# Kernel optimization log

Hardware: AMD Instinct MI355X
Metric: run time of the kernel (lower is better)

The kernel has to match this reference:

```python
import jax, jax.numpy as jnp
import numpy as np

LR = 0.1          # RMSprop learning rate (set_hyper_parameters)
ALPHA = 0.9       # RMSprop decay
ITERATIONS = 5    # SVGD iterations
INV_SIG2 = 1.0    # Gaussian posterior score scale (concrete post_grad)
EPS = 1e-8


def setup_inputs() -> dict:
    key = jax.random.key(0)
    k1, k2 = jax.random.split(key)
    x = jax.random.normal(k1, (8, 2048, 8), dtype=jnp.float32)          # [B, N, D] particles
    observation = jax.random.normal(k2, (8, 8), dtype=jnp.float32)      # [B, D]
    return {"x": x, "observation": observation}


def _svgd(x, observation):
    B, N, D = x.shape
    # median heuristic bandwidth h = median(pairwise dist)^2 / log(N), per batch, no-grad
    sq = jnp.sum((x[:, :, None, :] - x[:, None, :, :]) ** 2, axis=-1)   # [B, N, N]
    med = jnp.median(jnp.sqrt(sq).reshape(B, -1), axis=-1)              # [B]
    h = jax.lax.stop_gradient(med ** 2 / jnp.log(jnp.float32(N)))       # [B]
    inv_N = jnp.float32(1.0 / N)

    def post_grad(xc):
        # Gaussian posterior score: d/dx log N(x; observation, sigma^2 I)
        return (observation[:, None, :] - xc) * INV_SIG2                # [B, N, D]

    def step(carry, _):
        xc, s = carry
        dist = xc[:, :, None, :] - xc[:, None, :, :]                    # [B, i, j, D]
        K = jnp.exp(-jnp.sum(dist ** 2, axis=-1) / h[:, None, None])    # [B, i, j] rbf
        g = post_grad(xc)                                               # [B, j, D]
        # phi_i = (1/N) sum_j [ K_ij * g_j + (2/h)(x_i - x_j) K_ij ]
        phi = inv_N * (jnp.einsum('bij,bjd->bid', K, g)
                       + (2.0 / h)[:, None, None] * jnp.einsum('bij,bijd->bid', K, dist))
        # RMSprop (state update under no_grad in the original)
        s = jax.lax.stop_gradient(ALPHA * s + (1.0 - ALPHA) * phi ** 2)
        xc = xc + LR * phi / (jnp.sqrt(s) + EPS)
        return (xc, s), None

    (x, _), _ = jax.lax.scan(step, (x, jnp.zeros_like(x)), None, length=ITERATIONS)
    return x


def reference(x, observation):
    return _svgd(x, observation)
```

## Files before the change

kernel.cpp:

```cpp
#include <hip/hip_runtime.h>
#include <cstdint>

#define BATCH 8
#define NPART 2048
#define DDIM 8
#define NN (NPART * NPART)

#define MJCHUNK 256
#define SJCHUNK 512

constexpr float LR = 0.1f;
constexpr float ALPHA = 0.9f;
constexpr float EPS = 1e-8f;
constexpr float INV_N = 1.0f / (float)NPART;

typedef float v2f __attribute__((ext_vector_type(2)));
typedef float v4f __attribute__((ext_vector_type(4)));

__global__ __launch_bounds__(256) void init_ws_k(float* __restrict__ s,
                                                 unsigned* __restrict__ hist,
                                                 unsigned* __restrict__ prefix,
                                                 unsigned* __restrict__ rank) {
    const int tid = blockIdx.x * 256 + threadIdx.x;
    const int stride = gridDim.x * 256;
    for (int q = tid; q < BATCH * NPART * DDIM; q += stride) s[q] = 0.0f;
    if (tid < BATCH * 2 * 256) hist[tid] = 0u;
    if (tid < BATCH * 2) {
        prefix[tid] = 0u;
        rank[tid] = (unsigned)(NN / 2) + (unsigned)(tid & 1);
    }
}

__global__ __launch_bounds__(256) void median_hist_k(const float* __restrict__ x,
                                                     unsigned* __restrict__ hist,
                                                     const unsigned* __restrict__ prefix,
                                                     int shift) {
    __shared__ __align__(16) v4f xs0[MJCHUNK];
    __shared__ __align__(16) v4f xs1[MJCHUNK];
    __shared__ float rs[MJCHUNK];
    __shared__ unsigned lh[256 * 32];

    const int b = blockIdx.x;
    const int tid = threadIdx.x;
    const int slot = tid & 31;
    const float* xb = x + (size_t)b * NPART * DDIM;

    const unsigned p0 = prefix[2 * b + 0];
    const unsigned p1 = prefix[2 * b + 1];
    const bool same = (p0 == p1);
    const unsigned mask = (shift == 24) ? 0u : (0xFFFFFFFFu << (shift + 8));

    const int lane = tid & 15;
    const int trow = tid >> 4;
    const int ia = blockIdx.y * 32 + trow;
    const int ib = ia + 16;

    const v4f a0 = ((const v4f*)(xb + (size_t)ia * DDIM))[0];
    const v4f a1 = ((const v4f*)(xb + (size_t)ia * DDIM))[1];
    const v4f b0 = ((const v4f*)(xb + (size_t)ib * DDIM))[0];
    const v4f b1 = ((const v4f*)(xb + (size_t)ib * DDIM))[1];
    float qa = a0.x * a0.x + a0.y * a0.y + a0.z * a0.z + a0.w * a0.w
             + a1.x * a1.x + a1.y * a1.y + a1.z * a1.z + a1.w * a1.w;
    float qb = b0.x * b0.x + b0.y * b0.y + b0.z * b0.z + b0.w * b0.w
             + b1.x * b1.x + b1.y * b1.y + b1.z * b1.z + b1.w * b1.w;

    const int nsel = same ? 1 : 2;
    for (int sel = 0; sel < nsel; ++sel) {
        const unsigned pref = sel ? p1 : p0;
        __syncthreads();
        for (int t = tid; t < 256 * 32; t += 256) lh[t] = 0u;

        for (int cbase = 0; cbase < NPART; cbase += MJCHUNK) {
            __syncthreads();
            for (int t = tid; t < MJCHUNK; t += 256) {
                const v4f u0 = ((const v4f*)(xb + (size_t)(cbase + t) * DDIM))[0];
                const v4f u1 = ((const v4f*)(xb + (size_t)(cbase + t) * DDIM))[1];
                xs0[t] = u0;
                xs1[t] = u1;
                rs[t] = u0.x * u0.x + u0.y * u0.y + u0.z * u0.z + u0.w * u0.w
                      + u1.x * u1.x + u1.y * u1.y + u1.z * u1.z + u1.w * u1.w;
            }
            __syncthreads();
#pragma unroll 4
            for (int j = lane; j < MJCHUNK; j += 16) {
                const v4f A = xs0[j];
                const v4f B = xs1[j];
                const float r = rs[j];
                const v2f A0 = A.xy, A1 = A.zw, B0 = B.xy, B1 = B.zw;
                v2f p = A0 * a0.xy;
                p += A1 * a0.zw;
                p += B0 * a1.xy;
                p += B1 * a1.zw;
                float sq = fmaxf(fmaf(-2.0f, p.x + p.y, qa + r), 0.0f);
                unsigned u = __float_as_uint(sq);
                if ((u & mask) == pref)
                    atomicAdd(&lh[((u >> shift) & 255u) * 32 + slot], 1u);
                v2f q = A0 * b0.xy;
                q += A1 * b0.zw;
                q += B0 * b1.xy;
                q += B1 * b1.zw;
                sq = fmaxf(fmaf(-2.0f, q.x + q.y, qb + r), 0.0f);
                u = __float_as_uint(sq);
                if ((u & mask) == pref)
                    atomicAdd(&lh[((u >> shift) & 255u) * 32 + slot], 1u);
            }
        }
        __syncthreads();
        unsigned tot = 0;
#pragma unroll
        for (int sct = 0; sct < 32; ++sct) tot += lh[tid * 32 + ((sct + tid) & 31)];
        if (tot) {
            atomicAdd(&hist[b * 512 + sel * 256 + tid], tot);
            if (same) atomicAdd(&hist[b * 512 + 256 + tid], tot);
        }
    }
}

__global__ void median_scan_k(unsigned* __restrict__ hist,
                              unsigned* __restrict__ prefix,
                              unsigned* __restrict__ rank,
                              int shift,
                              float* __restrict__ hpar) {
    __shared__ unsigned selv[16];
    const int t = threadIdx.x;
    if (t < 16) {
        const unsigned r = rank[t];
        const unsigned* hb = hist + t * 256;
        unsigned cum = 0;
        int bin = 0;
        for (; bin < 256; ++bin) {
            const unsigned c = hb[bin];
            if (cum + c >= r) break;
            cum += c;
        }
        if (bin > 255) bin = 255;
        const unsigned np = prefix[t] | ((unsigned)bin << shift);
        prefix[t] = np;
        rank[t] = r - cum;
        selv[t] = np;
    }
    __syncthreads();
    for (int q = t; q < 16 * 256; q += 64) hist[q] = 0u;
    if (shift == 8 && t < BATCH) {
        const float v1 = __uint_as_float(selv[2 * t + 0]);
        const float v2 = __uint_as_float(selv[2 * t + 1]);
        const float med = 0.5f * (sqrtf(v1) + sqrtf(v2));
        const float h = (med * med) / logf((float)NPART);
        hpar[2 * t + 0] = -1.0f / h;
        hpar[2 * t + 1] = 2.0f / h;
    }
}

__global__ __launch_bounds__(256) void svgd_step_k(const float* __restrict__ x_in,
                                                   float* __restrict__ x_out,
                                                   float* __restrict__ s,
                                                   const float* __restrict__ hpar,
                                                   const float* __restrict__ obs) {
    __shared__ __align__(16) v4f xs0[SJCHUNK];
    __shared__ __align__(16) v4f xs1[SJCHUNK];
    __shared__ float rs[SJCHUNK];
    __shared__ float part[32][16][9];

    const int b = blockIdx.x;
    const int tid = threadIdx.x;
    const float* xb = x_in + (size_t)b * NPART * DDIM;

    const float nih = hpar[2 * b + 0];
    const float c2 = hpar[2 * b + 1];
    const float cdot = -2.0f * nih;

    const int lane = tid & 15;
    const int trow = tid >> 4;
    const int ia = blockIdx.y * 32 + trow;
    const int ib = ia + 16;

    const v4f a0 = ((const v4f*)(xb + (size_t)ia * DDIM))[0];
    const v4f a1 = ((const v4f*)(xb + (size_t)ia * DDIM))[1];
    const v4f b0 = ((const v4f*)(xb + (size_t)ib * DDIM))[0];
    const v4f b1 = ((const v4f*)(xb + (size_t)ib * DDIM))[1];
    const float qa = nih * (a0.x * a0.x + a0.y * a0.y + a0.z * a0.z + a0.w * a0.w
                          + a1.x * a1.x + a1.y * a1.y + a1.z * a1.z + a1.w * a1.w);
    const float qb = nih * (b0.x * b0.x + b0.y * b0.y + b0.z * b0.z + b0.w * b0.w
                          + b1.x * b1.x + b1.y * b1.y + b1.z * b1.z + b1.w * b1.w);

    float S0a = 0.0f, S0b = 0.0f;
    v2f Va0 = {0, 0}, Va1 = {0, 0}, Va2 = {0, 0}, Va3 = {0, 0};
    v2f Vb0 = {0, 0}, Vb1 = {0, 0}, Vb2 = {0, 0}, Vb3 = {0, 0};

    for (int cbase = 0; cbase < NPART; cbase += SJCHUNK) {
        __syncthreads();
        for (int t = tid; t < SJCHUNK; t += 256) {
            const v4f u0 = ((const v4f*)(xb + (size_t)(cbase + t) * DDIM))[0];
            const v4f u1 = ((const v4f*)(xb + (size_t)(cbase + t) * DDIM))[1];
            xs0[t] = u0;
            xs1[t] = u1;
            rs[t] = nih * (u0.x * u0.x + u0.y * u0.y + u0.z * u0.z + u0.w * u0.w
                         + u1.x * u1.x + u1.y * u1.y + u1.z * u1.z + u1.w * u1.w);
        }
        __syncthreads();
#pragma unroll 4
        for (int j = lane; j < SJCHUNK; j += 16) {
            const v4f A = xs0[j];
            const v4f B = xs1[j];
            const float r = rs[j];
            const v2f A0 = A.xy, A1 = A.zw, B0 = B.xy, B1 = B.zw;
            v2f p = A0 * a0.xy;
            p += A1 * a0.zw;
            p += B0 * a1.xy;
            p += B1 * a1.zw;
            const float Ka = __expf(fmaf(cdot, p.x + p.y, qa + r));
            S0a += Ka;
            const v2f Ka2 = {Ka, Ka};
            Va0 += A0 * Ka2;
            Va1 += A1 * Ka2;
            Va2 += B0 * Ka2;
            Va3 += B1 * Ka2;
            v2f q = A0 * b0.xy;
            q += A1 * b0.zw;
            q += B0 * b1.xy;
            q += B1 * b1.zw;
            const float Kb = __expf(fmaf(cdot, q.x + q.y, qb + r));
            S0b += Kb;
            const v2f Kb2 = {Kb, Kb};
            Vb0 += A0 * Kb2;
            Vb1 += A1 * Kb2;
            Vb2 += B0 * Kb2;
            Vb3 += B1 * Kb2;
        }
    }
    part[trow][lane][0] = S0a;
    part[trow][lane][1] = Va0.x;
    part[trow][lane][2] = Va0.y;
    part[trow][lane][3] = Va1.x;
    part[trow][lane][4] = Va1.y;
    part[trow][lane][5] = Va2.x;
    part[trow][lane][6] = Va2.y;
    part[trow][lane][7] = Va3.x;
    part[trow][lane][8] = Va3.y;
    part[trow + 16][lane][0] = S0b;
    part[trow + 16][lane][1] = Vb0.x;
    part[trow + 16][lane][2] = Vb0.y;
    part[trow + 16][lane][3] = Vb1.x;
    part[trow + 16][lane][4] = Vb1.y;
    part[trow + 16][lane][5] = Vb2.x;
    part[trow + 16][lane][6] = Vb2.y;
    part[trow + 16][lane][7] = Vb3.x;
    part[trow + 16][lane][8] = Vb3.y;
    __syncthreads();

    {
        const int d2i = tid & 7;
        const int r2 = tid >> 3;
        const int i2 = blockIdx.y * 32 + r2;
        float S0t = 0.0f, Vt = 0.0f;
#pragma unroll
        for (int l = 0; l < 16; ++l) {
            S0t += part[r2][l][0];
            Vt += part[r2][l][1 + d2i];
        }
        const size_t idx = ((size_t)b * NPART + i2) * DDIM + d2i;
        const float xid = x_in[idx];
        const float obsd = obs[b * DDIM + d2i];
        const float U = fmaf(S0t, xid, -Vt);
        const float T = fmaf(S0t, obsd - xid, U);
        const float phi = INV_N * fmaf(c2, U, T);
        float sv = s[idx];
        sv = ALPHA * sv + (1.0f - ALPHA) * phi * phi;
        s[idx] = sv;
        x_out[idx] = xid + LR * phi / (sqrtf(sv) + EPS);
    }
}

extern "C" void kernel_launch(void* const* d_in, const int* in_sizes, int n_in,
                              void* d_out, int out_size, void* d_ws, size_t ws_size,
                              hipStream_t stream) {
    const float* x0 = (const float*)d_in[0];
    const float* obs = (const float*)d_in[1];
    float* out = (float*)d_out;

    float* xa = (float*)d_ws;
    float* s = xa + BATCH * NPART * DDIM;
    unsigned* hist = (unsigned*)(s + BATCH * NPART * DDIM);
    unsigned* prefix = hist + BATCH * 2 * 256;
    unsigned* rank = prefix + BATCH * 2;
    float* hpar = (float*)(rank + BATCH * 2);

    init_ws_k<<<256, 256, 0, stream>>>(s, hist, prefix, rank);

    for (int r = 0; r < 3; ++r) {
        const int shift = 24 - 8 * r;
        median_hist_k<<<dim3(BATCH, 64), 256, 0, stream>>>(x0, hist, prefix, shift);
        median_scan_k<<<1, 64, 0, stream>>>(hist, prefix, rank, shift, hpar);
    }

    svgd_step_k<<<dim3(BATCH, 64), 256, 0, stream>>>(x0, out, s, hpar, obs);
    svgd_step_k<<<dim3(BATCH, 64), 256, 0, stream>>>(out, xa, s, hpar, obs);
    svgd_step_k<<<dim3(BATCH, 64), 256, 0, stream>>>(xa, out, s, hpar, obs);
    svgd_step_k<<<dim3(BATCH, 64), 256, 0, stream>>>(out, xa, s, hpar, obs);
    svgd_step_k<<<dim3(BATCH, 64), 256, 0, stream>>>(xa, out, s, hpar, obs);
}
```

Baseline: 230.0 us.

## Register-block four rows per thread in median and SVGD kernels, skip s zeroing

Each thread now holds four query particles in registers and strides the shared j-chunk by 32 lanes instead of two rows with 16 lanes. Every shared-memory load of a j particle is therefore reused across four i rows, which cuts LDS traffic per pair computed. The first SVGD step also starts RMSprop from zero state instead of reading s, so the init kernel no longer has to clear s. The cost is more registers per thread (16 accumulators of v2f plus xi) and a larger partial-reduction buffer in shared memory, which may lower occupancy.

Result: no change. 231.0 us (+0.4%).

```diff
diff --git a/kernel.cpp b/kernel.cpp
--- a/kernel.cpp
+++ b/kernel.cpp
@@ -17,13 +17,10 @@
 typedef float v2f __attribute__((ext_vector_type(2)));
 typedef float v4f __attribute__((ext_vector_type(4)));
 
-__global__ __launch_bounds__(256) void init_ws_k(float* __restrict__ s,
-                                                 unsigned* __restrict__ hist,
+__global__ __launch_bounds__(256) void init_ws_k(unsigned* __restrict__ hist,
                                                  unsigned* __restrict__ prefix,
                                                  unsigned* __restrict__ rank) {
     const int tid = blockIdx.x * 256 + threadIdx.x;
-    const int stride = gridDim.x * 256;
-    for (int q = tid; q < BATCH * NPART * DDIM; q += stride) s[q] = 0.0f;
     if (tid < BATCH * 2 * 256) hist[tid] = 0u;
     if (tid < BATCH * 2) {
         prefix[tid] = 0u;
@@ -42,7 +39,8 @@
 
     const int b = blockIdx.x;
     const int tid = threadIdx.x;
-    const int slot = tid & 31;
+    const int lane = tid & 31;
+    const int trow = tid >> 5;
     const float* xb = x + (size_t)b * NPART * DDIM;
 
     const unsigned p0 = prefix[2 * b + 0];
@@ -50,19 +48,18 @@
     const bool same = (p0 == p1);
     const unsigned mask = (shift == 24) ? 0u : (0xFFFFFFFFu << (shift + 8));
 
-    const int lane = tid & 15;
-    const int trow = tid >> 4;
-    const int ia = blockIdx.y * 32 + trow;
-    const int ib = ia + 16;
-
-    const v4f a0 = ((const v4f*)(xb + (size_t)ia * DDIM))[0];
-    const v4f a1 = ((const v4f*)(xb + (size_t)ia * DDIM))[1];
-    const v4f b0 = ((const v4f*)(xb + (size_t)ib * DDIM))[0];
-    const v4f b1 = ((const v4f*)(xb + (size_t)ib * DDIM))[1];
-    float qa = a0.x * a0.x + a0.y * a0.y + a0.z * a0.z + a0.w * a0.w
-             + a1.x * a1.x + a1.y * a1.y + a1.z * a1.z + a1.w * a1.w;
-    float qb = b0.x * b0.x + b0.y * b0.y + b0.z * b0.z + b0.w * b0.w
-             + b1.x * b1.x + b1.y * b1.y + b1.z * b1.z + b1.w * b1.w;
+    const int ibase = blockIdx.y * 32 + trow * 4;
+    v2f xi[4][4];
+    float q[4];
+#pragma unroll
+    for (int rr = 0; rr < 4; ++rr) {
+        const v4f t0 = ((const v4f*)(xb + (size_t)(ibase + rr) * DDIM))[0];
+        const v4f t1 = ((const v4f*)(xb + (size_t)(ibase + rr) * DDIM))[1];
+        xi[rr][0] = t0.xy; xi[rr][1] = t0.zw;
+        xi[rr][2] = t1.xy; xi[rr][3] = t1.zw;
+        q[rr] = t0.x * t0.x + t0.y * t0.y + t0.z * t0.z + t0.w * t0.w
+              + t1.x * t1.x + t1.y * t1.y + t1.z * t1.z + t1.w * t1.w;
+    }
 
     const int nsel = same ? 1 : 2;
     for (int sel = 0; sel < nsel; ++sel) {
@@ -81,28 +78,23 @@
                       + u1.x * u1.x + u1.y * u1.y + u1.z * u1.z + u1.w * u1.w;
             }
             __syncthreads();
-#pragma unroll 4
-            for (int j = lane; j < MJCHUNK; j += 16) {
+#pragma unroll 2
+            for (int j = lane; j < MJCHUNK; j += 32) {
                 const v4f A = xs0[j];
                 const v4f B = xs1[j];
                 const float r = rs[j];
                 const v2f A0 = A.xy, A1 = A.zw, B0 = B.xy, B1 = B.zw;
-                v2f p = A0 * a0.xy;
-                p += A1 * a0.zw;
-                p += B0 * a1.xy;
-                p += B1 * a1.zw;
-                float sq = fmaxf(fmaf(-2.0f, p.x + p.y, qa + r), 0.0f);
-                unsigned u = __float_as_uint(sq);
-                if ((u & mask) == pref)
-                    atomicAdd(&lh[((u >> shift) & 255u) * 32 + slot], 1u);
-                v2f q = A0 * b0.xy;
-                q += A1 * b0.zw;
-                q += B0 * b1.xy;
-                q += B1 * b1.zw;
-                sq = fmaxf(fmaf(-2.0f, q.x + q.y, qb + r), 0.0f);
-                u = __float_as_uint(sq);
-                if ((u & mask) == pref)
-                    atomicAdd(&lh[((u >> shift) & 255u) * 32 + slot], 1u);
+#pragma unroll
+                for (int rr = 0; rr < 4; ++rr) {
+                    v2f p = A0 * xi[rr][0];
+                    p += A1 * xi[rr][1];
+                    p += B0 * xi[rr][2];
+                    p += B1 * xi[rr][3];
+                    const float sq = fmaxf(fmaf(-2.0f, p.x + p.y, q[rr] + r), 0.0f);
+                    const unsigned u = __float_as_uint(sq);
+                    if ((u & mask) == pref)
+                        atomicAdd(&lh[((u >> shift) & 255u) * 32 + lane], 1u);
+                }
             }
         }
         __syncthreads();
@@ -155,37 +147,42 @@
                                                    float* __restrict__ x_out,
                                                    float* __restrict__ s,
                                                    const float* __restrict__ hpar,
-                                                   const float* __restrict__ obs) {
+                                                   const float* __restrict__ obs,
+                                                   int first) {
     __shared__ __align__(16) v4f xs0[SJCHUNK];
     __shared__ __align__(16) v4f xs1[SJCHUNK];
     __shared__ float rs[SJCHUNK];
-    __shared__ float part[32][16][9];
+    __shared__ float part[32][32][9];
 
     const int b = blockIdx.x;
     const int tid = threadIdx.x;
+    const int lane = tid & 31;
+    const int trow = tid >> 5;
     const float* xb = x_in + (size_t)b * NPART * DDIM;
 
     const float nih = hpar[2 * b + 0];
     const float c2 = hpar[2 * b + 1];
     const float cdot = -2.0f * nih;
 
-    const int lane = tid & 15;
-    const int trow = tid >> 4;
-    const int ia = blockIdx.y * 32 + trow;
-    const int ib = ia + 16;
-
-    const v4f a0 = ((const v4f*)(xb + (size_t)ia * DDIM))[0];
-    const v4f a1 = ((const v4f*)(xb + (size_t)ia * DDIM))[1];
-    const v4f b0 = ((const v4f*)(xb + (size_t)ib * DDIM))[0];
-    const v4f b1 = ((const v4f*)(xb + (size_t)ib * DDIM))[1];
-    const float qa = nih * (a0.x * a0.x + a0.y * a0.y + a0.z * a0.z + a0.w * a0.w
-                          + a1.x * a1.x + a1.y * a1.y + a1.z * a1.z + a1.w * a1.w);
-    const float qb = nih * (b0.x * b0.x + b0.y * b0.y + b0.z * b0.z + b0.w * b0.w
-                          + b1.x * b1.x + b1.y * b1.y + b1.z * b1.z + b1.w * b1.w);
-
-    float S0a = 0.0f, S0b = 0.0f;
-    v2f Va0 = {0, 0}, Va1 = {0, 0}, Va2 = {0, 0}, Va3 = {0, 0};
-    v2f Vb0 = {0, 0}, Vb1 = {0, 0}, Vb2 = {0, 0}, Vb3 = {0, 0};
+    const int ibase = blockIdx.y * 32 + trow * 4;
+    v2f xi[4][4];
+    float q[4];
+#pragma unroll
+    for (int rr = 0; rr < 4; ++rr) {
+        const v4f t0 = ((const v4f*)(xb + (size_t)(ibase + rr) * DDIM))[0];
+        const v4f t1 = ((const v4f*)(xb + (size_t)(ibase + rr) * DDIM))[1];
+        xi[rr][0] = t0.xy; xi[rr][1] = t0.zw;
+        xi[rr][2] = t1.xy; xi[rr][3] = t1.zw;
+        q[rr] = nih * (t0.x * t0.x + t0.y * t0.y + t0.z * t0.z + t0.w * t0.w
+                     + t1.x * t1.x + t1.y * t1.y + t1.z * t1.z + t1.w * t1.w);
+    }
+
+    float S0[4] = {0, 0, 0, 0};
+    v2f V[4][4];
+#pragma unroll
+    for (int rr = 0; rr < 4; ++rr)
+#pragma unroll
+        for (int k = 0; k < 4; ++k) V[rr][k] = (v2f){0, 0};
 
     for (int cbase = 0; cbase < NPART; cbase += SJCHUNK) {
         __syncthreads();
@@ -198,54 +195,41 @@
                          + u1.x * u1.x + u1.y * u1.y + u1.z * u1.z + u1.w * u1.w);
         }
         __syncthreads();
-#pragma unroll 4
-        for (int j = lane; j < SJCHUNK; j += 16) {
+#pragma unroll 2
+        for (int j = lane; j < SJCHUNK; j += 32) {
             const v4f A = xs0[j];
             const v4f B = xs1[j];
             const float r = rs[j];
             const v2f A0 = A.xy, A1 = A.zw, B0 = B.xy, B1 = B.zw;
-            v2f p = A0 * a0.xy;
-            p += A1 * a0.zw;
-            p += B0 * a1.xy;
-            p += B1 * a1.zw;
-            const float Ka = __expf(fmaf(cdot, p.x + p.y, qa + r));
-            S0a += Ka;
-            const v2f Ka2 = {Ka, Ka};
-            Va0 += A0 * Ka2;
-            Va1 += A1 * Ka2;
-            Va2 += B0 * Ka2;
-            Va3 += B1 * Ka2;
-            v2f q = A0 * b0.xy;
-            q += A1 * b0.zw;
-            q += B0 * b1.xy;
-            q += B1 * b1.zw;
-            const float Kb = __expf(fmaf(cdot, q.x + q.y, qb + r));
-            S0b += Kb;
-            const v2f Kb2 = {Kb, Kb};
-            Vb0 += A0 * Kb2;
-            Vb1 += A1 * Kb2;
-            Vb2 += B0 * Kb2;
-            Vb3 += B1 * Kb2;
-        }
-    }
-    part[trow][lane][0] = S0a;
-    part[trow][lane][1] = Va0.x;
-    part[trow][lane][2] = Va0.y;
-    part[trow][lane][3] = Va1.x;
-    part[trow][lane][4] = Va1.y;
-    part[trow][lane][5] = Va2.x;
-    part[trow][lane][6] = Va2.y;
-    part[trow][lane][7] = Va3.x;
-    part[trow][lane][8] = Va3.y;
-    part[trow + 16][lane][0] = S0b;
-    part[trow + 16][lane][1] = Vb0.x;
-    part[trow + 16][lane][2] = Vb0.y;
-    part[trow + 16][lane][3] = Vb1.x;
-    part[trow + 16][lane][4] = Vb1.y;
-    part[trow + 16][lane][5] = Vb2.x;
-    part[trow + 16][lane][6] = Vb2.y;
-    part[trow + 16][lane][7] = Vb3.x;
-    part[trow + 16][lane][8] = Vb3.y;
+#pragma unroll
+            for (int rr = 0; rr < 4; ++rr) {
+                v2f p = A0 * xi[rr][0];
+                p += A1 * xi[rr][1];
+                p += B0 * xi[rr][2];
+                p += B1 * xi[rr][3];
+                const float K = __expf(fmaf(cdot, p.x + p.y, q[rr] + r));
+                S0[rr] += K;
+                const v2f K2 = {K, K};
+                V[rr][0] += A0 * K2;
+                V[rr][1] += A1 * K2;
+                V[rr][2] += B0 * K2;
+                V[rr][3] += B1 * K2;
+            }
+        }
+    }
+#pragma unroll
+    for (int rr = 0; rr < 4; ++rr) {
+        const int row = trow * 4 + rr;
+        part[row][lane][0] = S0[rr];
+        part[row][lane][1] = V[rr][0].x;
+        part[row][lane][2] = V[rr][0].y;
+        part[row][lane][3] = V[rr][1].x;
+        part[row][lane][4] = V[rr][1].y;
+        part[row][lane][5] = V[rr][2].x;
+        part[row][lane][6] = V[rr][2].y;
+        part[row][lane][7] = V[rr][3].x;
+        part[row][lane][8] = V[rr][3].y;
+    }
     __syncthreads();
 
     {
@@ -254,7 +238,7 @@
         const int i2 = blockIdx.y * 32 + r2;
         float S0t = 0.0f, Vt = 0.0f;
 #pragma unroll
-        for (int l = 0; l < 16; ++l) {
+        for (int l = 0; l < 32; ++l) {
             S0t += part[r2][l][0];
             Vt += part[r2][l][1 + d2i];
         }
@@ -264,8 +248,12 @@
         const float U = fmaf(S0t, xid, -Vt);
         const float T = fmaf(S0t, obsd - xid, U);
         const float phi = INV_N * fmaf(c2, U, T);
-        float sv = s[idx];
-        sv = ALPHA * sv + (1.0f - ALPHA) * phi * phi;
+        float sv;
+        if (first) {
+            sv = (1.0f - ALPHA) * phi * phi;
+        } else {
+            sv = ALPHA * s[idx] + (1.0f - ALPHA) * phi * phi;
+        }
         s[idx] = sv;
         x_out[idx] = xid + LR * phi / (sqrtf(sv) + EPS);
     }
@@ -285,7 +273,7 @@
     unsigned* rank = prefix + BATCH * 2;
     float* hpar = (float*)(rank + BATCH * 2);
 
-    init_ws_k<<<256, 256, 0, stream>>>(s, hist, prefix, rank);
+    init_ws_k<<<16, 256, 0, stream>>>(hist, prefix, rank);
 
     for (int r = 0; r < 3; ++r) {
         const int shift = 24 - 8 * r;
@@ -293,9 +281,9 @@
         median_scan_k<<<1, 64, 0, stream>>>(hist, prefix, rank, shift, hpar);
     }
 
-    svgd_step_k<<<dim3(BATCH, 64), 256, 0, stream>>>(x0, out, s, hpar, obs);
-    svgd_step_k<<<dim3(BATCH, 64), 256, 0, stream>>>(out, xa, s, hpar, obs);
-    svgd_step_k<<<dim3(BATCH, 64), 256, 0, stream>>>(xa, out, s, hpar, obs);
-    svgd_step_k<<<dim3(BATCH, 64), 256, 0, stream>>>(out, xa, s, hpar, obs);
-    svgd_step_k<<<dim3(BATCH, 64), 256, 0, stream>>>(xa, out, s, hpar, obs);
-}
+    svgd_step_k<<<dim3(BATCH, 64), 256, 0, stream>>>(x0, out, s, hpar, obs, 1);
+    svgd_step_k<<<dim3(BATCH, 64), 256, 0, stream>>>(out, xa, s, hpar, obs, 0);
+    svgd_step_k<<<dim3(BATCH, 64), 256, 0, stream>>>(xa, out, s, hpar, obs, 0);
+    svgd_step_k<<<dim3(BATCH, 64), 256, 0, stream>>>(out, xa, s, hpar, obs, 0);
+    svgd_step_k<<<dim3(BATCH, 64), 256, 0, stream>>>(xa, out, s, hpar, obs, 0);
+}
```
